# Kernel tuning notes

Hardware: AMD Instinct MI355X
Metric: run time of the kernel (lower is better)

Reference implementation:

```python
import jax, jax.numpy as jnp
import numpy as np

B = 256       # batch
H = 512       # latent_size == hidden_size == t_channels == o_channels
O_LEN = 512   # decode steps (output_shape[0])


def setup_inputs() -> dict:
    key = jax.random.key(0)
    ks = jax.random.split(key, 7)
    s = 1.0 / np.sqrt(H)
    u = lambda k, shp: jax.random.uniform(k, shp, jnp.float32, -s, s)
    return {
        "z": jax.random.normal(ks[0], (B, H), jnp.float32),
        "W_ih": u(ks[1], (4 * H, H)),   # PyTorch LSTM weight_ih_l0, gate order i,f,g,o
        "W_hh": u(ks[2], (4 * H, H)),
        "b_ih": u(ks[3], (4 * H,)),
        "b_hh": u(ks[4], (4 * H,)),
        "W_last": u(ks[5], (H, H)),     # nn.Linear(hidden_size, o_channels)
        "b_last": u(ks[6], (H,)),
    }


def reference(z, W_ih, W_hh, b_ih, b_hh, W_last, b_last):
    b = b_ih + b_hh

    def step(carry, _):
        x, h, c = carry  # each (B, H)
        gates = x @ W_ih.T + h @ W_hh.T + b  # (B, 4H)
        i, f, g, o = jnp.split(gates, 4, axis=-1)
        c = jax.nn.sigmoid(f) * c + jax.nn.sigmoid(i) * jnp.tanh(g)
        h = jax.nn.sigmoid(o) * jnp.tanh(c)
        y = h @ W_last.T + b_last  # (B, H) -> fed back as next input
        return (y, h, c), y

    # state = (z, z) as (h0, c0); first input x0 = z
    _, ys = jax.lax.scan(step, (z, z, z), None, length=O_LEN)  # ys: (O_LEN, B, H)
    return jnp.transpose(ys, (1, 0, 2))  # (B, O_LEN, H)
```

## Files before the change

kernel.cpp:

```cpp
#include <hip/hip_runtime.h>


#define HH 512
#define TT 512

typedef _Float16 half8 __attribute__((ext_vector_type(8)));
typedef float f32x4 __attribute__((ext_vector_type(4)));

__device__ __forceinline__ float sigm(float x) { return 1.0f / (1.0f + __expf(-x)); }
__device__ __forceinline__ float tanh_(float x) { return 1.0f - 2.0f / (__expf(2.0f * x) + 1.0f); }
__device__ __forceinline__ unsigned short f16b(float x) {
    _Float16 h = (_Float16)x;
    return __builtin_bit_cast(unsigned short, h);
}

__global__ __launch_bounds__(256) void k_weff(const float* __restrict__ Wih,
                                              const float* __restrict__ Whh,
                                              const float* __restrict__ Wlast,
                                              unsigned short* __restrict__ Wbig) {
    __shared__ float wih[16 * 512];
    const int tid = threadIdx.x;
    const int r0 = blockIdx.x * 16;
    for (int i = tid; i < (16 * 512) / 4; i += 256) {
        ((float4*)wih)[i] = ((const float4*)(Wih + (size_t)r0 * 512))[i];
    }
    __syncthreads();
    float acc0[16], acc1[16];
#pragma unroll
    for (int rr = 0; rr < 16; ++rr) { acc0[rr] = 0.f; acc1[rr] = 0.f; }
    const int k0 = tid * 2;
    for (int j = 0; j < 512; ++j) {
        const float2 wl = *(const float2*)(Wlast + (size_t)j * 512 + k0);
#pragma unroll
        for (int rr = 0; rr < 16; ++rr) {
            const float a = wih[rr * 512 + j];
            acc0[rr] += a * wl.x;
            acc1[rr] += a * wl.y;
        }
    }
#pragma unroll
    for (int rr = 0; rr < 16; ++rr) {
        const int gr = r0 + rr;
        const int q = gr >> 9, j = gr & 511;
        const int dst = 80 * (j >> 4) + q * 16 + (j & 15);
        const float v0 = acc0[rr] + Whh[(size_t)gr * 512 + k0];
        const float v1 = acc1[rr] + Whh[(size_t)gr * 512 + k0 + 1];
        Wbig[(size_t)dst * 512 + k0] = f16b(v0);
        Wbig[(size_t)dst * 512 + k0 + 1] = f16b(v1);
    }
}

__global__ __launch_bounds__(256) void k_pack(const float* __restrict__ z,
                                              const float* __restrict__ Wih,
                                              const float* __restrict__ Whh,
                                              const float* __restrict__ bih,
                                              const float* __restrict__ bhh,
                                              const float* __restrict__ Wlast,
                                              const float* __restrict__ blast,
                                              unsigned short* __restrict__ Wbig,
                                              unsigned short* __restrict__ W0big,
                                              float* __restrict__ biasEff,
                                              float* __restrict__ bias0,
                                              unsigned short* __restrict__ hbuf,
                                              unsigned int* __restrict__ counters) {
    const int nthr = gridDim.x * blockDim.x;
    const int gtid = blockIdx.x * blockDim.x + threadIdx.x;
    for (int e = gtid; e < 2560 * 512; e += nthr) {
        const int r = e >> 9, k = e & 511;
        const int s = r / 80, rem = r - s * 80;
        const int tau = rem >> 4, jj = rem & 15;
        const int j = s * 16 + jj;
        if (tau == 4) {
            const unsigned short v = f16b(Wlast[(size_t)j * 512 + k]);
            Wbig[e] = v;
            W0big[e] = v;
        } else {
            const int gr = tau * 512 + j;
            W0big[e] = f16b(Wih[(size_t)gr * 512 + k] + Whh[(size_t)gr * 512 + k]);
        }
    }
    for (int r = gtid; r < 2560; r += nthr) {
        const int s = r / 80, rem = r - s * 80;
        const int tau = rem >> 4, jj = rem & 15;
        const int j = s * 16 + jj;
        if (tau == 4) {
            bias0[r] = blast[j];
            biasEff[r] = blast[j];
        } else {
            const int gr = tau * 512 + j;
            const float base = bih[gr] + bhh[gr];
            float dot = 0.f;
            for (int k = 0; k < 512; ++k) dot += Wih[(size_t)gr * 512 + k] * blast[k];
            bias0[r] = base;
            biasEff[r] = base + dot;
        }
    }
    for (int e = gtid; e < 256 * 512; e += nthr) {
        const int b = e >> 9, k = e & 511;
        const int g = b >> 4, bl = b & 15;
        hbuf[(size_t)g * 16384 + bl * 512 + k] = f16b(z[e]);
    }
    for (int e = gtid; e < 512; e += nthr) counters[e] = 0u;
}

__global__ __launch_bounds__(256, 1) void k_lstm(const unsigned short* __restrict__ Wbig,
                                                 const unsigned short* __restrict__ W0big,
                                                 const float* __restrict__ biasEff,
                                                 const float* __restrict__ bias0,
                                                 unsigned short* __restrict__ hbuf,
                                                 unsigned int* __restrict__ counters,
                                                 const float* __restrict__ z,
                                                 float* __restrict__ out) {
    const int g = blockIdx.x & 15;
    const int pair = blockIdx.x >> 4;
    const int tid = threadIdx.x;
    const int wave = tid >> 6;
    const int lane = tid & 63;
    const int l15 = lane & 15;
    const int q4 = lane >> 4;

    __shared__ unsigned short hstage[16 * 520];
    __shared__ float gatesL[2 * 16 * 68];
    __shared__ float cL[2 * 16 * 18];

    const int sl = wave >> 1;
    const int slice = 2 * pair + sl;
    const int ntile0 = (wave & 1) ? 3 : 0;
    const int ntcount = (wave & 1) ? 2 : 3;

    unsigned short* hb0 = hbuf + (size_t)g * 16384;
    unsigned short* hb1 = hb0 + 8192;
    unsigned int* cnt = counters + g * 32;

    for (int idx = tid; idx < 512; idx += 256) {
        const int b = idx >> 5, j0 = idx & 31;
        const int s2 = j0 >> 4, jj = j0 & 15;
        cL[(s2 * 16 + b) * 18 + jj] = z[(size_t)(g * 16 + b) * 512 + 32 * pair + j0];
    }

    half8 bfrag[3][16];
#pragma unroll
    for (int tt = 0; tt < 3; ++tt) {
        if (tt < ntcount) {
            const int row = 80 * slice + (ntile0 + tt) * 16 + l15;
#pragma unroll
            for (int kk = 0; kk < 16; ++kk) {
                bfrag[tt][kk] = *(const half8*)(W0big + (size_t)row * 512 + kk * 32 + q4 * 8);
            }
        }
    }
    float bias0v[3], biasEv[3];
#pragma unroll
    for (int tt = 0; tt < 3; ++tt) {
        if (tt < ntcount) {
            const int r = 80 * slice + (ntile0 + tt) * 16 + l15;
            bias0v[tt] = bias0[r];
            biasEv[tt] = biasEff[r];
        } else {
            bias0v[tt] = 0.f;
            biasEv[tt] = 0.f;
        }
    }

    for (int t = 0; t <= 512; ++t) {
        {
            const unsigned short* src = (t & 1) ? hb1 : hb0;
            const char* p = (const char*)src + tid * 16;
            half8 st[4];
            asm volatile(
                "global_load_dwordx4 %0, %4, off sc0 sc1\n\t"
                "global_load_dwordx4 %1, %5, off sc0 sc1\n\t"
                "global_load_dwordx4 %2, %6, off sc0 sc1\n\t"
                "global_load_dwordx4 %3, %7, off sc0 sc1\n\t"
                "s_waitcnt vmcnt(0)"
                : "=&v"(st[0]), "=&v"(st[1]), "=&v"(st[2]), "=&v"(st[3])
                : "v"(p), "v"(p + 4096), "v"(p + 8192), "v"(p + 12288)
                : "memory");
#pragma unroll
            for (int i = 0; i < 4; ++i) {
                const int ci = i * 256 + tid;
                const int row = ci >> 6, col = ci & 63;
                *(half8*)(hstage + row * 520 + col * 8) = st[i];
            }
        }
        __syncthreads();

        f32x4 acc[3];
#pragma unroll
        for (int tt = 0; tt < 3; ++tt) {
            const float bv = (t == 0) ? bias0v[tt] : biasEv[tt];
            acc[tt] = (f32x4){bv, bv, bv, bv};
        }
#pragma unroll
        for (int kk = 0; kk < 16; ++kk) {
            const half8 a = *(const half8*)(hstage + l15 * 520 + kk * 32 + q4 * 8);
#pragma unroll
            for (int tt = 0; tt < 3; ++tt) {
                if (tt < ntcount)
                    acc[tt] = __builtin_amdgcn_mfma_f32_16x16x32_f16(a, bfrag[tt][kk], acc[tt], 0, 0, 0);
            }
        }

        if ((wave & 1) && t >= 1) {
            const int n = 16 * slice + l15;
#pragma unroll
            for (int r = 0; r < 4; ++r) {
                const int m = q4 * 4 + r;
                const size_t off =
                    (size_t)(g * 16 + m) * (TT * HH) + (size_t)(t - 1) * HH + n;
                out[off] = acc[1][r];
            }
        }
        if (t == 512) break;

        {
            const int nst = (wave & 1) ? 1 : 3;
#pragma unroll
            for (int tt = 0; tt < 3; ++tt) {
                if (tt < nst) {
                    const int col = (ntile0 + tt) * 16 + l15;
#pragma unroll
                    for (int r = 0; r < 4; ++r) {
                        const int m = q4 * 4 + r;
                        gatesL[(sl * 16 + m) * 68 + col] = acc[tt][r];
                    }
                }
            }
        }
        __syncthreads();

        {
            const int b = tid >> 4, jp = tid & 15;
            const int j0 = jp * 2;
            const int s2 = j0 >> 4, jj = j0 & 15;
            const float* gb = gatesL + (s2 * 16 + b) * 68;
            const float2 iv = *(const float2*)(gb + jj);
            const float2 fvv = *(const float2*)(gb + 16 + jj);
            const float2 gv = *(const float2*)(gb + 32 + jj);
            const float2 ov = *(const float2*)(gb + 48 + jj);
            float* cp = cL + (s2 * 16 + b) * 18 + jj;
            float2 cv = *(const float2*)cp;
            const float c0 = sigm(fvv.x) * cv.x + sigm(iv.x) * tanh_(gv.x);
            const float c1 = sigm(fvv.y) * cv.y + sigm(iv.y) * tanh_(gv.y);
            const float h0 = sigm(ov.x) * tanh_(c0);
            const float h1 = sigm(ov.y) * tanh_(c1);
            cv.x = c0;
            cv.y = c1;
            *(float2*)cp = cv;
            unsigned short* dst = (t & 1) ? hb0 : hb1;
            const unsigned int packed = (unsigned int)f16b(h0) | ((unsigned int)f16b(h1) << 16);
            __hip_atomic_store((unsigned int*)(dst + b * 512 + 32 * pair + j0), packed,
                               __ATOMIC_RELAXED, __HIP_MEMORY_SCOPE_AGENT);
        }

        if (t == 0) {
#pragma unroll
            for (int tt = 0; tt < 3; ++tt) {
                if (tt < ntcount) {
                    const int row = 80 * slice + (ntile0 + tt) * 16 + l15;
#pragma unroll
                    for (int kk = 0; kk < 16; ++kk) {
                        bfrag[tt][kk] = *(const half8*)(Wbig + (size_t)row * 512 + kk * 32 + q4 * 8);
                    }
                }
            }
        }

        __syncthreads();
        if (tid == 0) {
            __hip_atomic_fetch_add(cnt, 1u, __ATOMIC_RELAXED, __HIP_MEMORY_SCOPE_AGENT);
            const unsigned int target = 16u * (unsigned)(t + 1);
            int guard = 0;
            while (__hip_atomic_load(cnt, __ATOMIC_RELAXED, __HIP_MEMORY_SCOPE_AGENT) < target &&
                   ++guard < 65536) {
            }
        }
        __syncthreads();
    }
}

extern "C" void kernel_launch(void* const* d_in, const int* in_sizes, int n_in,
                              void* d_out, int out_size, void* d_ws, size_t ws_size,
                              hipStream_t stream) {
    const float* z = (const float*)d_in[0];
    const float* Wih = (const float*)d_in[1];
    const float* Whh = (const float*)d_in[2];
    const float* bih = (const float*)d_in[3];
    const float* bhh = (const float*)d_in[4];
    const float* Wlast = (const float*)d_in[5];
    const float* blast = (const float*)d_in[6];
    float* out = (float*)d_out;

    char* ws = (char*)d_ws;
    unsigned short* Wbig = (unsigned short*)(ws);
    unsigned short* W0big = (unsigned short*)(ws + 2621440);
    float* biasEff = (float*)(ws + 5242880);
    float* bias0 = (float*)(ws + 5253120);
    unsigned short* hbuf = (unsigned short*)(ws + 5263360);
    unsigned int* counters = (unsigned int*)(ws + 5787648);

    k_weff<<<128, 256, 0, stream>>>(Wih, Whh, Wlast, Wbig);
    k_pack<<<512, 256, 0, stream>>>(z, Wih, Whh, bih, bhh, Wlast, blast, Wbig, W0big, biasEff,
                                    bias0, hbuf, counters);
    k_lstm<<<256, 256, 0, stream>>>(Wbig, W0big, biasEff, bias0, hbuf, counters, z, out);
}
```

Measured before the change: 2.026 ms.

## Replace atomic counter barrier with sequence-tagged hidden-state flags

```diff
diff --git a/kernel.cpp b/kernel.cpp
--- a/kernel.cpp
+++ b/kernel.cpp
@@ -6,6 +6,8 @@
 
 typedef _Float16 half8 __attribute__((ext_vector_type(8)));
 typedef float f32x4 __attribute__((ext_vector_type(4)));
+typedef unsigned int u32x2 __attribute__((ext_vector_type(2)));
+typedef unsigned int u32x4 __attribute__((ext_vector_type(4)));
 
 __device__ __forceinline__ float sigm(float x) { return 1.0f / (1.0f + __expf(-x)); }
 __device__ __forceinline__ float tanh_(float x) { return 1.0f - 2.0f / (__expf(2.0f * x) + 1.0f); }
@@ -61,8 +63,7 @@
                                               unsigned short* __restrict__ W0big,
                                               float* __restrict__ biasEff,
                                               float* __restrict__ bias0,
-                                              unsigned short* __restrict__ hbuf,
-                                              unsigned int* __restrict__ counters) {
+                                              unsigned int* __restrict__ hbuf32) {
     const int nthr = gridDim.x * blockDim.x;
     const int gtid = blockIdx.x * blockDim.x + threadIdx.x;
     for (int e = gtid; e < 2560 * 512; e += nthr) {
@@ -98,17 +99,17 @@
     for (int e = gtid; e < 256 * 512; e += nthr) {
         const int b = e >> 9, k = e & 511;
         const int g = b >> 4, bl = b & 15;
-        hbuf[(size_t)g * 16384 + bl * 512 + k] = f16b(z[e]);
-    }
-    for (int e = gtid; e < 512; e += nthr) counters[e] = 0u;
+        unsigned int* base = hbuf32 + (size_t)g * 16384 + bl * 512 + k;
+        base[0] = ((unsigned int)f16b(z[e]) << 16);
+        base[8192] = 0xFFFFFFFFu;
+    }
 }
 
 __global__ __launch_bounds__(256, 1) void k_lstm(const unsigned short* __restrict__ Wbig,
                                                  const unsigned short* __restrict__ W0big,
                                                  const float* __restrict__ biasEff,
                                                  const float* __restrict__ bias0,
-                                                 unsigned short* __restrict__ hbuf,
-                                                 unsigned int* __restrict__ counters,
+                                                 unsigned int* __restrict__ hbuf32,
                                                  const float* __restrict__ z,
                                                  float* __restrict__ out) {
     const int g = blockIdx.x & 15;
@@ -128,9 +129,7 @@
     const int ntile0 = (wave & 1) ? 3 : 0;
     const int ntcount = (wave & 1) ? 2 : 3;
 
-    unsigned short* hb0 = hbuf + (size_t)g * 16384;
-    unsigned short* hb1 = hb0 + 8192;
-    unsigned int* cnt = counters + g * 32;
+    unsigned int* hbg = hbuf32 + (size_t)g * 16384;
 
     for (int idx = tid; idx < 512; idx += 256) {
         const int b = idx >> 5, j0 = idx & 31;
@@ -164,23 +163,48 @@
 
     for (int t = 0; t <= 512; ++t) {
         {
-            const unsigned short* src = (t & 1) ? hb1 : hb0;
-            const char* p = (const char*)src + tid * 16;
-            half8 st[4];
-            asm volatile(
-                "global_load_dwordx4 %0, %4, off sc0 sc1\n\t"
-                "global_load_dwordx4 %1, %5, off sc0 sc1\n\t"
-                "global_load_dwordx4 %2, %6, off sc0 sc1\n\t"
-                "global_load_dwordx4 %3, %7, off sc0 sc1\n\t"
-                "s_waitcnt vmcnt(0)"
-                : "=&v"(st[0]), "=&v"(st[1]), "=&v"(st[2]), "=&v"(st[3])
-                : "v"(p), "v"(p + 4096), "v"(p + 8192), "v"(p + 12288)
-                : "memory");
-#pragma unroll
-            for (int i = 0; i < 4; ++i) {
+            const unsigned int seqt = (unsigned int)t;
+            unsigned int* bufp = hbg + ((t & 1) ? 8192 : 0);
+            u32x4 st[8];
+            bool valid[8] = {false, false, false, false, false, false, false, false};
+            int pass = 0;
+            while (true) {
+#pragma unroll
+                for (int i = 0; i < 8; ++i) {
+                    if (!valid[i]) {
+                        const char* p = (const char*)bufp + (i * 256 + tid) * 16;
+                        asm volatile("global_load_dwordx4 %0, %1, off sc0 sc1"
+                                     : "=&v"(st[i])
+                                     : "v"(p)
+                                     : "memory");
+                    }
+                }
+                asm volatile("s_waitcnt vmcnt(0)"
+                             : "+v"(st[0]), "+v"(st[1]), "+v"(st[2]), "+v"(st[3]),
+                               "+v"(st[4]), "+v"(st[5]), "+v"(st[6]), "+v"(st[7])
+                             :
+                             : "memory");
+                bool all = true;
+#pragma unroll
+                for (int i = 0; i < 8; ++i) {
+                    if (!valid[i]) {
+                        valid[i] = ((st[i][0] & 0xFFFFu) == seqt) & ((st[i][1] & 0xFFFFu) == seqt) &
+                                   ((st[i][2] & 0xFFFFu) == seqt) & ((st[i][3] & 0xFFFFu) == seqt);
+                    }
+                    all = all & valid[i];
+                }
+                if (__ballot(!all) == 0ull) break;
+                if (++pass >= 8192) break;
+            }
+#pragma unroll
+            for (int i = 0; i < 8; ++i) {
                 const int ci = i * 256 + tid;
-                const int row = ci >> 6, col = ci & 63;
-                *(half8*)(hstage + row * 520 + col * 8) = st[i];
+                const int row = ci >> 7;
+                const int colw = (ci & 127) * 4;
+                u32x2 pk;
+                pk.x = (st[i][0] >> 16) | (st[i][1] & 0xFFFF0000u);
+                pk.y = (st[i][2] >> 16) | (st[i][3] & 0xFFFF0000u);
+                *(u32x2*)(hstage + row * 520 + colw) = pk;
             }
         }
         __syncthreads();
@@ -206,8 +230,7 @@
 #pragma unroll
             for (int r = 0; r < 4; ++r) {
                 const int m = q4 * 4 + r;
-                const size_t off =
-                    (size_t)(g * 16 + m) * (TT * HH) + (size_t)(t - 1) * HH + n;
+                const size_t off = (size_t)(g * 16 + m) * (TT * HH) + (size_t)(t - 1) * HH + n;
                 out[off] = acc[1][r];
             }
         }
@@ -247,10 +270,14 @@
             cv.x = c0;
             cv.y = c1;
             *(float2*)cp = cv;
-            unsigned short* dst = (t & 1) ? hb0 : hb1;
-            const unsigned int packed = (unsigned int)f16b(h0) | ((unsigned int)f16b(h1) << 16);
-            __hip_atomic_store((unsigned int*)(dst + b * 512 + 32 * pair + j0), packed,
-                               __ATOMIC_RELAXED, __HIP_MEMORY_SCOPE_AGENT);
+            const unsigned int seq1 = (unsigned int)(t + 1);
+            unsigned int* dstp =
+                hbg + (((t + 1) & 1) ? 8192 : 0) + b * 512 + 32 * pair + j0;
+            u32x2 w2;
+            w2.x = ((unsigned int)f16b(h0) << 16) | seq1;
+            w2.y = ((unsigned int)f16b(h1) << 16) | seq1;
+            asm volatile("global_store_dwordx2 %0, %1, off sc0 sc1" ::"v"(dstp), "v"(w2)
+                         : "memory");
         }
 
         if (t == 0) {
@@ -265,17 +292,6 @@
                 }
             }
         }
-
-        __syncthreads();
-        if (tid == 0) {
-            __hip_atomic_fetch_add(cnt, 1u, __ATOMIC_RELAXED, __HIP_MEMORY_SCOPE_AGENT);
-            const unsigned int target = 16u * (unsigned)(t + 1);
-            int guard = 0;
-            while (__hip_atomic_load(cnt, __ATOMIC_RELAXED, __HIP_MEMORY_SCOPE_AGENT) < target &&
-                   ++guard < 65536) {
-            }
-        }
-        __syncthreads();
     }
 }
 
@@ -296,11 +312,10 @@
     unsigned short* W0big = (unsigned short*)(ws + 2621440);
     float* biasEff = (float*)(ws + 5242880);
     float* bias0 = (float*)(ws + 5253120);
-    unsigned short* hbuf = (unsigned short*)(ws + 5263360);
-    unsigned int* counters = (unsigned int*)(ws + 5787648);
+    unsigned int* hbuf32 = (unsigned int*)(ws + 5263360);
 
     k_weff<<<128, 256, 0, stream>>>(Wih, Whh, Wlast, Wbig);
     k_pack<<<512, 256, 0, stream>>>(z, Wih, Whh, bih, bhh, Wlast, blast, Wbig, W0big, biasEff,
-                                    bias0, hbuf, counters);
-    k_lstm<<<256, 256, 0, stream>>>(Wbig, W0big, biasEff, bias0, hbuf, counters, z, out);
-}
+                                    bias0, hbuf32);
+    k_lstm<<<256, 256, 0, stream>>>(Wbig, W0big, biasEff, bias0, hbuf32, z, out);
+}
```

After: 2.915 ms. 1.44x slower.
